# Kernel tuning notes

Measured on AMD Instinct MI355X. Metric: run time of the kernel, lower is better.

The kernel has to match this reference:

```python
import jax, jax.numpy as jnp
import numpy as np

TEMPERATURE = 8.0


def setup_inputs() -> dict:
    key = jax.random.key(0)
    kq, kk, kv, km = jax.random.split(key, 4)
    B, H, S, D = 2, 16, 2048, 64
    q = jax.random.normal(kq, (B, H, S, D), dtype=jnp.float32)
    k = jax.random.normal(kk, (B, H, S, D), dtype=jnp.float32)
    v = jax.random.normal(kv, (B, H, S, D), dtype=jnp.float32)
    mask = jax.random.randint(km, (B, S, S), 0, 2, dtype=jnp.int32)
    return {"q": q, "k": k, "v": v, "mask": mask}


def reference(q, k, v, mask):
    # attn = q @ k^T / temperature  -> [B,H,Sq,Sk]
    attn = jnp.einsum("bhqd,bhkd->bhqk", q, k) / TEMPERATURE
    # mask: [B,Sq,Sk] -> [B,1,Sq,Sk]; masked where mask == 0
    m0 = (mask == 0)[:, None, :, :]
    attn = jnp.where(m0, -jnp.inf, attn)
    attn = jax.nn.softmax(attn, axis=-1)
    attn = jnp.where(m0, 0.0, attn)
    output = jnp.einsum("bhqk,bhkd->bhqd", attn, v)
    return (output, attn)
```

## Files before the change

### kernel.cpp

```cpp
#include <hip/hip_runtime.h>


#define S 2048
#define D 64
#define HH 16
#define BB 2
#define NE (BB * HH * S * D)

typedef __attribute__((ext_vector_type(8))) short short8;
typedef __attribute__((ext_vector_type(4))) float f32x4;
typedef __attribute__((ext_vector_type(2))) unsigned int u32x2;

__device__ __forceinline__ unsigned int packbf2(float a, float b) {
  union { __bf16 h[2]; unsigned int u; } r;
  r.h[0] = (__bf16)a;
  r.h[1] = (__bf16)b;
  return r.u;
}
__device__ __forceinline__ short8 cvt8(float4 a, float4 b) {
  union { unsigned int u[4]; short8 s; } r;
  r.u[0] = packbf2(a.x, a.y); r.u[1] = packbf2(a.z, a.w);
  r.u[2] = packbf2(b.x, b.y); r.u[3] = packbf2(b.z, b.w);
  return r.s;
}
#define QSC 0.1803368801111204f
__device__ __forceinline__ float4 qscale(float4 v) {
  return make_float4(v.x * QSC, v.y * QSC, v.z * QSC, v.w * QSC);
}
__device__ __forceinline__ float exp2fast(float x) {
  float r;
  asm("v_exp_f32 %0, %1" : "=v"(r) : "v"(x));
  return r;
}

#define TRRD(dst, addr, off) \
  asm volatile("ds_read_b64_tr_b16 %0, %1 offset:" #off : "=v"(dst) : "v"(addr))

__global__ __launch_bounds__(256) void pack_mask_kernel(
    const int* __restrict__ m, unsigned long long* __restrict__ bits) {
  int wid = blockIdx.x * 4 + (threadIdx.x >> 6);
  int lane = threadIdx.x & 63;
  int v = m[(size_t)wid * 64 + lane];
  unsigned long long b = __ballot(v != 0);
  if (lane == 0) bits[wid] = b;
}

__global__ __launch_bounds__(256) void cvt_kv_kernel(
    const float* __restrict__ K, const float* __restrict__ V,
    unsigned short* __restrict__ Kb, unsigned short* __restrict__ Vb) {
  size_t i = ((size_t)blockIdx.x * 256 + threadIdx.x) * 8;
  const float* s;
  unsigned short* d;
  if (i < (size_t)NE) { s = K + i; d = Kb + i; }
  else { s = V + (i - NE); d = Vb + (i - NE); }
  float4 a = *reinterpret_cast<const float4*>(s);
  float4 b = *reinterpret_cast<const float4*>(s + 4);
  *reinterpret_cast<short8*>(d) = cvt8(a, b);
}

template <int PRE>
__global__ __launch_bounds__(256) void attn_kernel(
    const float* __restrict__ Qg, const void* __restrict__ Kx,
    const void* __restrict__ Vx, const unsigned long long* __restrict__ Mb,
    float* __restrict__ Og, float* __restrict__ Ag) {
  __shared__ alignas(128) unsigned short Vt[2][4096];

  const int tid = threadIdx.x;
  const int w = tid >> 6;
  const int lane = tid & 63;
  const int ln15 = lane & 15;
  const int quad = lane >> 4;

  const int bh = blockIdx.x;
  const int qtile = blockIdx.y;
  const int b = bh >> 4;
  const size_t qkvbase = (size_t)bh * S * D;
  const int q0 = qtile * 64;
  const int qrow = q0 + w * 16 + ln15;

  const float4* qp = reinterpret_cast<const float4*>(Qg + qkvbase + (size_t)qrow * D);
  short8 aq0, aq1;
  {
    float4 a0 = qscale(qp[quad * 2]), a1 = qscale(qp[quad * 2 + 1]);
    float4 b0 = qscale(qp[8 + quad * 2]), b1 = qscale(qp[8 + quad * 2 + 1]);
    aq0 = cvt8(a0, a1);
    aq1 = cvt8(b0, b1);
  }

  const unsigned long long* mrow = Mb + ((size_t)b * S + qrow) * (S / 64);

  const unsigned short* pkh =
      reinterpret_cast<const unsigned short*>(Kx) + qkvbase + (size_t)ln15 * D + quad * 8;
  const float* pkf =
      reinterpret_cast<const float*>(Kx) + qkvbase + (size_t)ln15 * D + quad * 8;

  auto loadK = [&](int row, short8& b0, short8& b1) {
    if constexpr (PRE) {
      const unsigned short* p = pkh + (size_t)row * D;
      b0 = *reinterpret_cast<const short8*>(p);
      b1 = *reinterpret_cast<const short8*>(p + 32);
    } else {
      const float* p = pkf + (size_t)row * D;
      float4 a0 = *reinterpret_cast<const float4*>(p);
      float4 a1 = *reinterpret_cast<const float4*>(p + 4);
      float4 c0 = *reinterpret_cast<const float4*>(p + 32);
      float4 c1 = *reinterpret_cast<const float4*>(p + 36);
      b0 = cvt8(a0, a1);
      b1 = cvt8(c0, c1);
    }
  };

  float lsum = 0.f;
#pragma unroll 2
  for (int t = 0; t < 32; ++t) {
    unsigned long long mw = mrow[t];
#pragma unroll
    for (int kt = 0; kt < 4; ++kt) {
      short8 bk0, bk1;
      loadK(t * 64 + kt * 16, bk0, bk1);
      f32x4 acc = {0.f, 0.f, 0.f, 0.f};
      acc = __builtin_amdgcn_mfma_f32_16x16x32_bf16(bk0, aq0, acc, 0, 0, 0);
      acc = __builtin_amdgcn_mfma_f32_16x16x32_bf16(bk1, aq1, acc, 0, 0, 0);
      unsigned int nib = (unsigned int)(mw >> (kt * 16 + quad * 4)) & 0xFu;
#pragma unroll
      for (int r = 0; r < 4; ++r) {
        float e = exp2fast(acc[r]);
        lsum += ((nib >> r) & 1u) ? e : 0.f;
      }
    }
  }
  lsum += __shfl_xor(lsum, 16, 64);
  lsum += __shfl_xor(lsum, 32, 64);
  const float rinv = (lsum > 0.f) ? 1.f / lsum : 0.f;

  float* arow = Ag + ((size_t)bh * S + qrow) * S;
  f32x4 oacc[4] = {{0.f, 0.f, 0.f, 0.f}, {0.f, 0.f, 0.f, 0.f},
                   {0.f, 0.f, 0.f, 0.f}, {0.f, 0.f, 0.f, 0.f}};

  const int trow = tid >> 2;
  const int d0c = (tid & 3) << 4;
  const int vwoff = ((trow >> 2) * 4 + (tid & 3)) * 64 + (trow & 3) * 16;
  const unsigned int vb0 =
      (unsigned int)(unsigned long long)(const void*)&Vt[0][0] +
      (unsigned int)(quad * 512 + ln15 * 8);

  const unsigned short* pvh =
      reinterpret_cast<const unsigned short*>(Vx) + qkvbase + (size_t)trow * D + d0c;
  const float* pvf =
      reinterpret_cast<const float*>(Vx) + qkvbase + (size_t)trow * D + d0c;

  short8 hv0, hv1;
  float4 fv0, fv1, fv2, fv3;
  auto loadV = [&](int t) {
    if constexpr (PRE) {
      const unsigned short* p = pvh + (size_t)t * 64 * D;
      hv0 = *reinterpret_cast<const short8*>(p);
      hv1 = *reinterpret_cast<const short8*>(p + 8);
    } else {
      const float* p = pvf + (size_t)t * 64 * D;
      fv0 = reinterpret_cast<const float4*>(p)[0];
      fv1 = reinterpret_cast<const float4*>(p)[1];
      fv2 = reinterpret_cast<const float4*>(p)[2];
      fv3 = reinterpret_cast<const float4*>(p)[3];
    }
  };
  auto writeV = [&](int buf) {
    unsigned short* dst = &Vt[buf][vwoff];
    if constexpr (PRE) {
      *reinterpret_cast<short8*>(dst) = hv0;
      *reinterpret_cast<short8*>(dst + 8) = hv1;
    } else {
      *reinterpret_cast<short8*>(dst) = cvt8(fv0, fv1);
      *reinterpret_cast<short8*>(dst + 8) = cvt8(fv2, fv3);
    }
  };

  loadV(0);
  writeV(0);
  loadV(1);
  __syncthreads();

  for (int t = 0; t < 32; ++t) {
    const int cur = t & 1;
    if (t < 31) writeV(cur ^ 1);
    if (t < 30) loadV(t + 2);
    unsigned long long mw = mrow[t];
    const int k0 = t * 64;
    unsigned int apu[8];
#pragma unroll
    for (int kt = 0; kt < 4; ++kt) {
      short8 bk0, bk1;
      loadK(t * 64 + kt * 16, bk0, bk1);
      f32x4 acc = {0.f, 0.f, 0.f, 0.f};
      acc = __builtin_amdgcn_mfma_f32_16x16x32_bf16(bk0, aq0, acc, 0, 0, 0);
      acc = __builtin_amdgcn_mfma_f32_16x16x32_bf16(bk1, aq1, acc, 0, 0, 0);
      unsigned int nib = (unsigned int)(mw >> (kt * 16 + quad * 4)) & 0xFu;
      f32x4 p;
#pragma unroll
      for (int r = 0; r < 4; ++r) {
        float e = exp2fast(acc[r]) * rinv;
        p[r] = ((nib >> r) & 1u) ? e : 0.f;
      }
      __builtin_nontemporal_store(p, reinterpret_cast<f32x4*>(arow + k0 + kt * 16 + quad * 4));
      apu[kt * 2] = packbf2(p[0], p[1]);
      apu[kt * 2 + 1] = packbf2(p[2], p[3]);
    }
    const unsigned int vb = vb0 + (unsigned int)(cur << 13);
    u32x2 x0, x1, x2, x3, x4, x5, x6, x7, x8, x9, x10, x11, x12, x13, x14, x15;
    TRRD(x0, vb, 0);     TRRD(x1, vb, 2048);
    TRRD(x2, vb, 128);   TRRD(x3, vb, 2176);
    TRRD(x4, vb, 256);   TRRD(x5, vb, 2304);
    TRRD(x6, vb, 384);   TRRD(x7, vb, 2432);
    TRRD(x8, vb, 4096);  TRRD(x9, vb, 6144);
    TRRD(x10, vb, 4224); TRRD(x11, vb, 6272);
    TRRD(x12, vb, 4352); TRRD(x13, vb, 6400);
    TRRD(x14, vb, 4480); TRRD(x15, vb, 6528);
    asm volatile("s_waitcnt lgkmcnt(0)" ::: "memory");
    __builtin_amdgcn_sched_barrier(0);
    union Frag { unsigned int u[4]; u32x2 d[2]; short8 s; };
    Frag ap0, ap1, bv;
    ap0.u[0] = apu[0]; ap0.u[1] = apu[1]; ap0.u[2] = apu[2]; ap0.u[3] = apu[3];
    ap1.u[0] = apu[4]; ap1.u[1] = apu[5]; ap1.u[2] = apu[6]; ap1.u[3] = apu[7];
    bv.d[0] = x0;  bv.d[1] = x1;
    oacc[0] = __builtin_amdgcn_mfma_f32_16x16x32_bf16(ap0.s, bv.s, oacc[0], 0, 0, 0);
    bv.d[0] = x2;  bv.d[1] = x3;
    oacc[1] = __builtin_amdgcn_mfma_f32_16x16x32_bf16(ap0.s, bv.s, oacc[1], 0, 0, 0);
    bv.d[0] = x4;  bv.d[1] = x5;
    oacc[2] = __builtin_amdgcn_mfma_f32_16x16x32_bf16(ap0.s, bv.s, oacc[2], 0, 0, 0);
    bv.d[0] = x6;  bv.d[1] = x7;
    oacc[3] = __builtin_amdgcn_mfma_f32_16x16x32_bf16(ap0.s, bv.s, oacc[3], 0, 0, 0);
    bv.d[0] = x8;  bv.d[1] = x9;
    oacc[0] = __builtin_amdgcn_mfma_f32_16x16x32_bf16(ap1.s, bv.s, oacc[0], 0, 0, 0);
    bv.d[0] = x10; bv.d[1] = x11;
    oacc[1] = __builtin_amdgcn_mfma_f32_16x16x32_bf16(ap1.s, bv.s, oacc[1], 0, 0, 0);
    bv.d[0] = x12; bv.d[1] = x13;
    oacc[2] = __builtin_amdgcn_mfma_f32_16x16x32_bf16(ap1.s, bv.s, oacc[2], 0, 0, 0);
    bv.d[0] = x14; bv.d[1] = x15;
    oacc[3] = __builtin_amdgcn_mfma_f32_16x16x32_bf16(ap1.s, bv.s, oacc[3], 0, 0, 0);
    __syncthreads();
  }

#pragma unroll
  for (int c = 0; c < 4; ++c) {
#pragma unroll
    for (int r = 0; r < 4; ++r) {
      Og[qkvbase + (size_t)(q0 + w * 16 + quad * 4 + r) * D + c * 16 + ln15] = oacc[c][r];
    }
  }
}

extern "C" void kernel_launch(void* const* d_in, const int* in_sizes, int n_in,
                              void* d_out, int out_size, void* d_ws, size_t ws_size,
                              hipStream_t stream) {
  const float* q = (const float*)d_in[0];
  const float* k = (const float*)d_in[1];
  const float* v = (const float*)d_in[2];
  const int* m = (const int*)d_in[3];
  float* outp = (float*)d_out;
  float* attnp = outp + (size_t)BB * HH * S * D;

  const size_t bitsBytes = (size_t)BB * S * (S / 64) * 8;
  unsigned long long* bits = (unsigned long long*)d_ws;
  unsigned short* Kb = (unsigned short*)((char*)d_ws + bitsBytes);
  unsigned short* Vb = Kb + (size_t)NE;
  const bool pre = ws_size >= bitsBytes + 2 * (size_t)NE * sizeof(unsigned short);

  const int nwords = BB * S * (S / 64);
  pack_mask_kernel<<<nwords / 4, 256, 0, stream>>>(m, bits);
  dim3 grid(BB * HH, S / 64);
  if (pre) {
    cvt_kv_kernel<<<(2 * (size_t)NE / 8) / 256, 256, 0, stream>>>(k, v, Kb, Vb);
    attn_kernel<1><<<grid, 256, 0, stream>>>(q, Kb, Vb, bits, outp, attnp);
  } else {
    attn_kernel<0><<<grid, 256, 0, stream>>>(q, k, v, bits, outp, attnp);
  }
}
```

Measured before the change: 846.4 us.

## Stage V via global_load_lds, batch K loads, drop nontemporal stores, set MFMA prio

Result: no change. 838.8 us (-0.9%).

```diff
diff --git a/kernel.cpp b/kernel.cpp
--- a/kernel.cpp
+++ b/kernel.cpp
@@ -31,6 +31,11 @@
   float r;
   asm("v_exp_f32 %0, %1" : "=v"(r) : "v"(x));
   return r;
+}
+__device__ __forceinline__ void gload_lds16(const void* g, void* l) {
+  __builtin_amdgcn_global_load_lds(
+      (const __attribute__((address_space(1))) void*)g,
+      (__attribute__((address_space(3))) void*)l, 16, 0, 0);
 }
 
 #define TRRD(dst, addr, off) \
@@ -114,13 +119,14 @@
 #pragma unroll 2
   for (int t = 0; t < 32; ++t) {
     unsigned long long mw = mrow[t];
+    short8 bk[4][2];
+#pragma unroll
+    for (int kt = 0; kt < 4; ++kt) loadK(t * 64 + kt * 16, bk[kt][0], bk[kt][1]);
 #pragma unroll
     for (int kt = 0; kt < 4; ++kt) {
-      short8 bk0, bk1;
-      loadK(t * 64 + kt * 16, bk0, bk1);
       f32x4 acc = {0.f, 0.f, 0.f, 0.f};
-      acc = __builtin_amdgcn_mfma_f32_16x16x32_bf16(bk0, aq0, acc, 0, 0, 0);
-      acc = __builtin_amdgcn_mfma_f32_16x16x32_bf16(bk1, aq1, acc, 0, 0, 0);
+      acc = __builtin_amdgcn_mfma_f32_16x16x32_bf16(bk[kt][0], aq0, acc, 0, 0, 0);
+      acc = __builtin_amdgcn_mfma_f32_16x16x32_bf16(bk[kt][1], aq1, acc, 0, 0, 0);
       unsigned int nib = (unsigned int)(mw >> (kt * 16 + quad * 4)) & 0xFu;
 #pragma unroll
       for (int r = 0; r < 4; ++r) {
@@ -137,63 +143,54 @@
   f32x4 oacc[4] = {{0.f, 0.f, 0.f, 0.f}, {0.f, 0.f, 0.f, 0.f},
                    {0.f, 0.f, 0.f, 0.f}, {0.f, 0.f, 0.f, 0.f}};
 
+  const int i0 = w * 64 + lane;
+  const int i1 = 256 + w * 64 + lane;
+  const int so0 = (i0 >> 5) * 256 + ((i0 >> 1) & 3) * 64 + ((i0 >> 3) & 3) * 16 + (i0 & 1) * 8;
+  const int so1 = (i1 >> 5) * 256 + ((i1 >> 1) & 3) * 64 + ((i1 >> 3) & 3) * 16 + (i1 & 1) * 8;
+  const unsigned short* pvh = reinterpret_cast<const unsigned short*>(Vx) + qkvbase;
+
   const int trow = tid >> 2;
   const int d0c = (tid & 3) << 4;
   const int vwoff = ((trow >> 2) * 4 + (tid & 3)) * 64 + (trow & 3) * 16;
+  const float* pvf = reinterpret_cast<const float*>(Vx) + qkvbase + (size_t)trow * D + d0c;
+
+  auto stage = [&](int buf, int t) {
+    if constexpr (PRE) {
+      const unsigned short* src = pvh + (size_t)t * (64 * D);
+      gload_lds16(src + so0, &Vt[buf][w * 512]);
+      gload_lds16(src + so1, &Vt[buf][2048 + w * 512]);
+    } else {
+      const float* p = pvf + (size_t)t * 64 * D;
+      float4 a0 = reinterpret_cast<const float4*>(p)[0];
+      float4 a1 = reinterpret_cast<const float4*>(p)[1];
+      float4 a2 = reinterpret_cast<const float4*>(p)[2];
+      float4 a3 = reinterpret_cast<const float4*>(p)[3];
+      *reinterpret_cast<short8*>(&Vt[buf][vwoff]) = cvt8(a0, a1);
+      *reinterpret_cast<short8*>(&Vt[buf][vwoff + 8]) = cvt8(a2, a3);
+    }
+  };
+
+  stage(0, 0);
+  __syncthreads();
+
   const unsigned int vb0 =
       (unsigned int)(unsigned long long)(const void*)&Vt[0][0] +
       (unsigned int)(quad * 512 + ln15 * 8);
 
-  const unsigned short* pvh =
-      reinterpret_cast<const unsigned short*>(Vx) + qkvbase + (size_t)trow * D + d0c;
-  const float* pvf =
-      reinterpret_cast<const float*>(Vx) + qkvbase + (size_t)trow * D + d0c;
-
-  short8 hv0, hv1;
-  float4 fv0, fv1, fv2, fv3;
-  auto loadV = [&](int t) {
-    if constexpr (PRE) {
-      const unsigned short* p = pvh + (size_t)t * 64 * D;
-      hv0 = *reinterpret_cast<const short8*>(p);
-      hv1 = *reinterpret_cast<const short8*>(p + 8);
-    } else {
-      const float* p = pvf + (size_t)t * 64 * D;
-      fv0 = reinterpret_cast<const float4*>(p)[0];
-      fv1 = reinterpret_cast<const float4*>(p)[1];
-      fv2 = reinterpret_cast<const float4*>(p)[2];
-      fv3 = reinterpret_cast<const float4*>(p)[3];
-    }
-  };
-  auto writeV = [&](int buf) {
-    unsigned short* dst = &Vt[buf][vwoff];
-    if constexpr (PRE) {
-      *reinterpret_cast<short8*>(dst) = hv0;
-      *reinterpret_cast<short8*>(dst + 8) = hv1;
-    } else {
-      *reinterpret_cast<short8*>(dst) = cvt8(fv0, fv1);
-      *reinterpret_cast<short8*>(dst + 8) = cvt8(fv2, fv3);
-    }
-  };
-
-  loadV(0);
-  writeV(0);
-  loadV(1);
-  __syncthreads();
-
   for (int t = 0; t < 32; ++t) {
     const int cur = t & 1;
-    if (t < 31) writeV(cur ^ 1);
-    if (t < 30) loadV(t + 2);
+    if (t < 31) stage(cur ^ 1, t + 1);
     unsigned long long mw = mrow[t];
     const int k0 = t * 64;
+    short8 bk[4][2];
+#pragma unroll
+    for (int kt = 0; kt < 4; ++kt) loadK(t * 64 + kt * 16, bk[kt][0], bk[kt][1]);
     unsigned int apu[8];
 #pragma unroll
     for (int kt = 0; kt < 4; ++kt) {
-      short8 bk0, bk1;
-      loadK(t * 64 + kt * 16, bk0, bk1);
       f32x4 acc = {0.f, 0.f, 0.f, 0.f};
-      acc = __builtin_amdgcn_mfma_f32_16x16x32_bf16(bk0, aq0, acc, 0, 0, 0);
-      acc = __builtin_amdgcn_mfma_f32_16x16x32_bf16(bk1, aq1, acc, 0, 0, 0);
+      acc = __builtin_amdgcn_mfma_f32_16x16x32_bf16(bk[kt][0], aq0, acc, 0, 0, 0);
+      acc = __builtin_amdgcn_mfma_f32_16x16x32_bf16(bk[kt][1], aq1, acc, 0, 0, 0);
       unsigned int nib = (unsigned int)(mw >> (kt * 16 + quad * 4)) & 0xFu;
       f32x4 p;
 #pragma unroll
@@ -201,7 +198,7 @@
         float e = exp2fast(acc[r]) * rinv;
         p[r] = ((nib >> r) & 1u) ? e : 0.f;
       }
-      __builtin_nontemporal_store(p, reinterpret_cast<f32x4*>(arow + k0 + kt * 16 + quad * 4));
+      *reinterpret_cast<f32x4*>(arow + k0 + kt * 16 + quad * 4) = p;
       apu[kt * 2] = packbf2(p[0], p[1]);
       apu[kt * 2 + 1] = packbf2(p[2], p[3]);
     }
@@ -221,6 +218,7 @@
     Frag ap0, ap1, bv;
     ap0.u[0] = apu[0]; ap0.u[1] = apu[1]; ap0.u[2] = apu[2]; ap0.u[3] = apu[3];
     ap1.u[0] = apu[4]; ap1.u[1] = apu[5]; ap1.u[2] = apu[6]; ap1.u[3] = apu[7];
+    __builtin_amdgcn_s_setprio(1);
     bv.d[0] = x0;  bv.d[1] = x1;
     oacc[0] = __builtin_amdgcn_mfma_f32_16x16x32_bf16(ap0.s, bv.s, oacc[0], 0, 0, 0);
     bv.d[0] = x2;  bv.d[1] = x3;
@@ -237,6 +235,7 @@
     oacc[2] = __builtin_amdgcn_mfma_f32_16x16x32_bf16(ap1.s, bv.s, oacc[2], 0, 0, 0);
     bv.d[0] = x14; bv.d[1] = x15;
     oacc[3] = __builtin_amdgcn_mfma_f32_16x16x32_bf16(ap1.s, bv.s, oacc[3], 0, 0, 0);
+    __builtin_amdgcn_s_setprio(0);
     __syncthreads();
   }
 
```
